# Performance work log

Measured on AMD Instinct MI355X. Metric: run time of the kernel, lower is better.

Reference implementation:

```python
import jax, jax.numpy as jnp
import numpy as np

N_NODES = 1048576
N_GRAPHS = 1024
F_X = 128
F_U = 128
HIDDEN = 512
F_U_OUT = 128
N_EDGES = 4096
F_E = 128


def setup_inputs() -> dict:
    key = jax.random.key(0)
    ks = jax.random.split(key, 8)
    x = jax.random.normal(ks[0], (N_NODES, F_X), dtype=jnp.float32)
    edge_index = jax.random.randint(ks[1], (2, N_EDGES), 0, N_NODES, dtype=jnp.int64)
    edge_attr = jax.random.normal(ks[2], (N_EDGES, F_E), dtype=jnp.float32)
    u = jax.random.normal(ks[3], (N_GRAPHS, F_U), dtype=jnp.float32)
    batch = jnp.sort(jax.random.randint(ks[4], (N_NODES,), 0, N_GRAPHS, dtype=jnp.int64))
    W1 = jax.random.normal(ks[5], (F_X + F_U, HIDDEN), dtype=jnp.float32) * (1.0 / np.sqrt(F_X + F_U))
    b1 = jnp.zeros((HIDDEN,), dtype=jnp.float32)
    W2 = jax.random.normal(ks[6], (HIDDEN, F_U_OUT), dtype=jnp.float32) * (1.0 / np.sqrt(HIDDEN))
    b2 = jnp.zeros((F_U_OUT,), dtype=jnp.float32)
    return {"x": x, "edge_index": edge_index, "edge_attr": edge_attr, "u": u,
            "batch": batch, "W1": W1, "b1": b1, "W2": W2, "b2": b2}


def reference(x, edge_index, edge_attr, u, batch, W1, b1, W2, b2):
    # scatter_mean(x, batch, dim=0): per-graph mean of node features.
    sums = jax.ops.segment_sum(x, batch, num_segments=N_GRAPHS)          # [B, f_x]
    counts = jax.ops.segment_sum(jnp.ones((x.shape[0],), x.dtype), batch,
                                 num_segments=N_GRAPHS)                  # [B]
    x_agg = sums / jnp.maximum(counts, 1.0)[:, None]                     # empty segs -> 0
    out = jnp.concatenate([x_agg, u], axis=1)                            # [B, f_x+f_u]
    h = jax.nn.relu(out @ W1 + b1)                                       # [B, hidden]
    return h @ W2 + b2                                                   # [B, f_u_out]
```

## Files before the change

### kernel.cpp

```cpp
#include <hip/hip_runtime.h>

#define N_NODES   1048576
#define N_GRAPHS  1024
#define F_XDIM    128
#define F_UDIM    128
#define HIDDEN    512
#define F_OUT     128
#define ROWS_PER_BLOCK 256

__global__ __launch_bounds__(256) void seg_invcount_kernel(
        const int* __restrict__ batch, float* __restrict__ inv_cnt) {
    int g = blockIdx.x * blockDim.x + threadIdx.x;
    if (g >= N_GRAPHS) return;
    auto lb = [&](int target) {
        int lo = 0, hi = N_NODES;
        while (lo < hi) {
            int mid = (lo + hi) >> 1;
            if (batch[mid] < target) lo = mid + 1; else hi = mid;
        }
        return lo;
    };
    int c = lb(g + 1) - lb(g);
    inv_cnt[g] = 1.0f / (float)max(c, 1);
}

__global__ __launch_bounds__(256) void seg_sum_kernel(
        const float* __restrict__ x, const int* __restrict__ batch,
        float* __restrict__ sums) {
    const int grp  = threadIdx.x >> 5;
    const int lane = threadIdx.x & 31;
    const int row0 = blockIdx.x * ROWS_PER_BLOCK;

    float4 acc = make_float4(0.f, 0.f, 0.f, 0.f);
    int cur = -1;

    for (int r = row0 + grp; r < row0 + ROWS_PER_BLOCK; r += 8) {
        int seg = batch[r];
        float4 v = reinterpret_cast<const float4*>(x + (size_t)r * F_XDIM)[lane];
        if (seg != cur) {
            if (cur >= 0) {
                float* dst = sums + (size_t)cur * F_XDIM + lane * 4;
                atomicAdd(dst + 0, acc.x);
                atomicAdd(dst + 1, acc.y);
                atomicAdd(dst + 2, acc.z);
                atomicAdd(dst + 3, acc.w);
            }
            cur = seg;
            acc = v;
        } else {
            acc.x += v.x; acc.y += v.y; acc.z += v.z; acc.w += v.w;
        }
    }
    if (cur >= 0) {
        float* dst = sums + (size_t)cur * F_XDIM + lane * 4;
        atomicAdd(dst + 0, acc.x);
        atomicAdd(dst + 1, acc.y);
        atomicAdd(dst + 2, acc.z);
        atomicAdd(dst + 3, acc.w);
    }
}

#define GT 4
__global__ __launch_bounds__(256) void mlp_kernel(
        const float* __restrict__ sums, const float* __restrict__ inv_cnt,
        const float* __restrict__ u,
        const float* __restrict__ W1, const float* __restrict__ b1,
        const float* __restrict__ W2, const float* __restrict__ b2,
        float* __restrict__ out) {
    __shared__ float in_s[GT][F_XDIM + F_UDIM];
    __shared__ float h_s[GT][HIDDEN];

    const int t  = threadIdx.x;
    const int g0 = blockIdx.x * GT;

    for (int g = 0; g < GT; ++g) {
        float v;
        if (t < F_XDIM) v = sums[(size_t)(g0 + g) * F_XDIM + t] * inv_cnt[g0 + g];
        else            v = u[(size_t)(g0 + g) * F_UDIM + (t - F_XDIM)];
        in_s[g][t] = v;
    }
    __syncthreads();

    float acc0[GT], acc1[GT];
    {
        float bb0 = b1[t], bb1 = b1[t + 256];
        #pragma unroll
        for (int g = 0; g < GT; ++g) { acc0[g] = bb0; acc1[g] = bb1; }
    }
    for (int k = 0; k < F_XDIM + F_UDIM; ++k) {
        float w0 = W1[(size_t)k * HIDDEN + t];
        float w1 = W1[(size_t)k * HIDDEN + t + 256];
        #pragma unroll
        for (int g = 0; g < GT; ++g) {
            float iv = in_s[g][k];
            acc0[g] = fmaf(iv, w0, acc0[g]);
            acc1[g] = fmaf(iv, w1, acc1[g]);
        }
    }
    #pragma unroll
    for (int g = 0; g < GT; ++g) {
        h_s[g][t]       = fmaxf(acc0[g], 0.f);
        h_s[g][t + 256] = fmaxf(acc1[g], 0.f);
    }
    __syncthreads();

    const int c  = t & 127;
    const int gp = (t >> 7) * 2;
    float y0 = b2[c], y1 = b2[c];
    for (int k = 0; k < HIDDEN; ++k) {
        float w = W2[(size_t)k * F_OUT + c];
        y0 = fmaf(h_s[gp][k],     w, y0);
        y1 = fmaf(h_s[gp + 1][k], w, y1);
    }
    out[(size_t)(g0 + gp)     * F_OUT + c] = y0;
    out[(size_t)(g0 + gp + 1) * F_OUT + c] = y1;
}

extern "C" void kernel_launch(void* const* d_in, const int* in_sizes, int n_in,
                              void* d_out, int out_size, void* d_ws, size_t ws_size,
                              hipStream_t stream) {
    const float* x     = (const float*)d_in[0];
    const float* u     = (const float*)d_in[3];
    const int*   batch = (const int*)  d_in[4];
    const float* W1    = (const float*)d_in[5];
    const float* b1    = (const float*)d_in[6];
    const float* W2    = (const float*)d_in[7];
    const float* b2    = (const float*)d_in[8];
    float* out = (float*)d_out;

    float* sums    = (float*)d_ws;
    float* inv_cnt = sums + N_GRAPHS * F_XDIM;

    hipMemsetAsync(sums, 0, N_GRAPHS * F_XDIM * sizeof(float), stream);

    seg_invcount_kernel<<<(N_GRAPHS + 255) / 256, 256, 0, stream>>>(batch, inv_cnt);
    seg_sum_kernel<<<N_NODES / ROWS_PER_BLOCK, 256, 0, stream>>>(x, batch, sums);
    mlp_kernel<<<N_GRAPHS / GT, 256, 0, stream>>>(sums, inv_cnt, u, W1, b1, W2, b2, out);
}
```

Baseline: 798.7 us.

## Replace atomic segment sum with per-graph block reduction via binary search

```diff
diff --git a/kernel.cpp b/kernel.cpp
--- a/kernel.cpp
+++ b/kernel.cpp
@@ -6,64 +6,50 @@
 #define F_UDIM    128
 #define HIDDEN    512
 #define F_OUT     128
-#define ROWS_PER_BLOCK 256
 
-__global__ __launch_bounds__(256) void seg_invcount_kernel(
-        const int* __restrict__ batch, float* __restrict__ inv_cnt) {
-    int g = blockIdx.x * blockDim.x + threadIdx.x;
-    if (g >= N_GRAPHS) return;
-    auto lb = [&](int target) {
-        int lo = 0, hi = N_NODES;
-        while (lo < hi) {
-            int mid = (lo + hi) >> 1;
-            if (batch[mid] < target) lo = mid + 1; else hi = mid;
-        }
-        return lo;
-    };
-    int c = lb(g + 1) - lb(g);
-    inv_cnt[g] = 1.0f / (float)max(c, 1);
-}
+__global__ __launch_bounds__(512) void seg_mean_kernel(
+        const float* __restrict__ x, const int* __restrict__ batch,
+        float* __restrict__ x_agg) {
+    const int g    = blockIdx.x;
+    const int t    = threadIdx.x;
+    const int grp  = t >> 5;
+    const int lane = t & 31;
 
-__global__ __launch_bounds__(256) void seg_sum_kernel(
-        const float* __restrict__ x, const int* __restrict__ batch,
-        float* __restrict__ sums) {
-    const int grp  = threadIdx.x >> 5;
-    const int lane = threadIdx.x & 31;
-    const int row0 = blockIdx.x * ROWS_PER_BLOCK;
+    int lo = 0, hi = N_NODES;
+    while (lo < hi) {
+        int mid = (lo + hi) >> 1;
+        if (batch[mid] < g) lo = mid + 1; else hi = mid;
+    }
+    const int s = lo;
+    hi = N_NODES;
+    while (lo < hi) {
+        int mid = (lo + hi) >> 1;
+        if (batch[mid] < g + 1) lo = mid + 1; else hi = mid;
+    }
+    const int e = lo;
 
     float4 acc = make_float4(0.f, 0.f, 0.f, 0.f);
-    int cur = -1;
+    for (int r = s + grp; r < e; r += 16) {
+        float4 v = reinterpret_cast<const float4*>(x + (size_t)r * F_XDIM)[lane];
+        acc.x += v.x; acc.y += v.y; acc.z += v.z; acc.w += v.w;
+    }
 
-    for (int r = row0 + grp; r < row0 + ROWS_PER_BLOCK; r += 8) {
-        int seg = batch[r];
-        float4 v = reinterpret_cast<const float4*>(x + (size_t)r * F_XDIM)[lane];
-        if (seg != cur) {
-            if (cur >= 0) {
-                float* dst = sums + (size_t)cur * F_XDIM + lane * 4;
-                atomicAdd(dst + 0, acc.x);
-                atomicAdd(dst + 1, acc.y);
-                atomicAdd(dst + 2, acc.z);
-                atomicAdd(dst + 3, acc.w);
-            }
-            cur = seg;
-            acc = v;
-        } else {
-            acc.x += v.x; acc.y += v.y; acc.z += v.z; acc.w += v.w;
-        }
-    }
-    if (cur >= 0) {
-        float* dst = sums + (size_t)cur * F_XDIM + lane * 4;
-        atomicAdd(dst + 0, acc.x);
-        atomicAdd(dst + 1, acc.y);
-        atomicAdd(dst + 2, acc.z);
-        atomicAdd(dst + 3, acc.w);
+    __shared__ float partial[16][F_XDIM];
+    reinterpret_cast<float4*>(&partial[grp][lane * 4])[0] = acc;
+    __syncthreads();
+
+    if (t < F_XDIM) {
+        float m = 0.f;
+        #pragma unroll
+        for (int j = 0; j < 16; ++j) m += partial[j][t];
+        const float inv = 1.0f / (float)max(e - s, 1);
+        x_agg[(size_t)g * F_XDIM + t] = m * inv;
     }
 }
 
 #define GT 4
 __global__ __launch_bounds__(256) void mlp_kernel(
-        const float* __restrict__ sums, const float* __restrict__ inv_cnt,
-        const float* __restrict__ u,
+        const float* __restrict__ x_agg, const float* __restrict__ u,
         const float* __restrict__ W1, const float* __restrict__ b1,
         const float* __restrict__ W2, const float* __restrict__ b2,
         float* __restrict__ out) {
@@ -75,7 +61,7 @@
 
     for (int g = 0; g < GT; ++g) {
         float v;
-        if (t < F_XDIM) v = sums[(size_t)(g0 + g) * F_XDIM + t] * inv_cnt[g0 + g];
+        if (t < F_XDIM) v = x_agg[(size_t)(g0 + g) * F_XDIM + t];
         else            v = u[(size_t)(g0 + g) * F_UDIM + (t - F_XDIM)];
         in_s[g][t] = v;
     }
@@ -128,12 +114,8 @@
     const float* b2    = (const float*)d_in[8];
     float* out = (float*)d_out;
 
-    float* sums    = (float*)d_ws;
-    float* inv_cnt = sums + N_GRAPHS * F_XDIM;
+    float* x_agg = (float*)d_ws;
 
-    hipMemsetAsync(sums, 0, N_GRAPHS * F_XDIM * sizeof(float), stream);
-
-    seg_invcount_kernel<<<(N_GRAPHS + 255) / 256, 256, 0, stream>>>(batch, inv_cnt);
-    seg_sum_kernel<<<N_NODES / ROWS_PER_BLOCK, 256, 0, stream>>>(x, batch, sums);
-    mlp_kernel<<<N_GRAPHS / GT, 256, 0, stream>>>(sums, inv_cnt, u, W1, b1, W2, b2, out);
+    seg_mean_kernel<<<N_GRAPHS, 512, 0, stream>>>(x, batch, x_agg);
+    mlp_kernel<<<N_GRAPHS / GT, 256, 0, stream>>>(x_agg, u, W1, b1, W2, b2, out);
 }
```

New measurement: 752.3 us. -5.8%, faster.
